# Optimization experiments

Hardware: AMD Instinct MI355X
Metric: run time of the kernel (lower is better)

Reference implementation:

```python
import jax, jax.numpy as jnp
import numpy as np

S = 8192          # total tokens (8 images x 1024 patches)
DIM = 1280        # hidden_size
H = 16            # num_heads
DH = DIM // H     # head_dim = 80
N_SEG = 8         # number of image segments (equal-length)


def setup_inputs() -> dict:
    key = jax.random.key(0)
    ks = jax.random.split(key, 8)
    hidden_states = jax.random.normal(ks[0], (S, DIM), dtype=jnp.float32)
    ang = jax.random.uniform(ks[1], (S, DH), dtype=jnp.float32) * (2.0 * np.pi)
    cos = jnp.cos(ang)
    sin = jnp.sin(ang)
    cu_seqlens = (jnp.arange(N_SEG + 1, dtype=jnp.int32) * (S // N_SEG))
    qkv_w = jax.random.normal(ks[2], (3 * DIM, DIM), dtype=jnp.float32) * 0.02
    qkv_b = jax.random.normal(ks[3], (3 * DIM,), dtype=jnp.float32) * 0.02
    proj_w = jax.random.normal(ks[4], (DIM, DIM), dtype=jnp.float32) * 0.02
    proj_b = jax.random.normal(ks[5], (DIM,), dtype=jnp.float32) * 0.02
    return {
        "hidden_states": hidden_states,
        "cos": cos,
        "sin": sin,
        "qkv_w": qkv_w,
        "qkv_b": qkv_b,
        "proj_w": proj_w,
        "proj_b": proj_b,
        "cu_seqlens": cu_seqlens,
    }


def _rotate_half(x):
    d = x.shape[-1] // 2
    return jnp.concatenate([-x[..., d:], x[..., :d]], axis=-1)


def reference(hidden_states, cos, sin, qkv_w, qkv_b, proj_w, proj_b, cu_seqlens):
    s, dim = hidden_states.shape
    dh = cos.shape[-1]
    h = dim // dh
    n_seg = cu_seqlens.shape[0] - 1  # static; segments are equal-length
    L = s // n_seg
    scale = dh ** -0.5

    # fused QKV projection: [S, 3, H, DH]
    qkv = (hidden_states @ qkv_w.T + qkv_b).reshape(s, 3, h, dh)
    q, k, v = qkv[:, 0], qkv[:, 1], qkv[:, 2]

    # RoPE (fp32, broadcast cos/sin over heads)
    cos_b = cos[:, None, :].astype(jnp.float32)
    sin_b = sin[:, None, :].astype(jnp.float32)
    qf, kf = q.astype(jnp.float32), k.astype(jnp.float32)
    q = (qf * cos_b + _rotate_half(qf) * sin_b).astype(q.dtype)
    k = (kf * cos_b + _rotate_half(kf) * sin_b).astype(k.dtype)

    # per-segment (block-diagonal) attention: reshape to [n_seg, L, H, DH]
    qs = q.reshape(n_seg, L, h, dh)
    ks = k.reshape(n_seg, L, h, dh)
    vs = v.reshape(n_seg, L, h, dh)
    scores = jnp.einsum("glhd,gmhd->ghlm", qs, ks) * scale
    attn = jax.nn.softmax(scores, axis=-1)
    out = jnp.einsum("ghlm,gmhd->glhd", attn, vs).reshape(s, dim)
    return out @ proj_w.T + proj_b
```

## Files before the change

### kernel.cpp

```cpp
#include <hip/hip_runtime.h>
#include <hip/hip_bf16.h>
#include <stdint.h>

typedef unsigned short u16;
typedef unsigned int u32;
typedef __attribute__((ext_vector_type(8))) short short8;
typedef __attribute__((ext_vector_type(4))) float f32x4;

#define DEV __device__ __forceinline__

constexpr int S = 8192;
constexpr int DIM = 1280;
constexpr int H = 16;
constexpr int DH = 80;
constexpr int LSEG = 1024;
constexpr int QKVN = 3 * DIM;
constexpr float SCALE = 0.11180339887498949f * 1.4426950408889634f;

DEV u16 f2bf(float f) {
  u32 u = __float_as_uint(f);
  return (u16)((u + 0x7FFFu + ((u >> 16) & 1u)) >> 16);
}
DEV float bf2f(u16 h) { return __uint_as_float(((u32)h) << 16); }
DEV u32 pkbf(float a, float b) {
  __hip_bfloat162 t = __float22bfloat162_rn(float2{a, b});
  u32 r; __builtin_memcpy(&r, &t, 4); return r;
}

DEV void glds16(const void* g, void* l) {
  __builtin_amdgcn_global_load_lds((__attribute__((address_space(1))) void*)g,
                                   (__attribute__((address_space(3))) void*)l,
                                   16, 0, 0);
}
DEV f32x4 mfma16(short8 a, short8 b, f32x4 c) {
  return __builtin_amdgcn_mfma_f32_16x16x32_bf16(a, b, c, 0, 0, 0);
}

__global__ __launch_bounds__(256) void cvt_kernel(
    const float* __restrict__ X, const float* __restrict__ Wq,
    const float* __restrict__ Wp, u16* __restrict__ Xb,
    u16* __restrict__ Wqb, u16* __restrict__ Wpb) {
  size_t i = ((size_t)blockIdx.x * 256 + threadIdx.x) * 4;
  const size_t n1 = (size_t)S * DIM;
  const size_t n2 = (size_t)QKVN * DIM;
  const size_t n3 = (size_t)DIM * DIM;
  const float* src; u16* dst; size_t off;
  if (i < n1)                { src = X;  dst = Xb;  off = i; }
  else if (i < n1 + n2)      { src = Wq; dst = Wqb; off = i - n1; }
  else if (i < n1 + n2 + n3) { src = Wp; dst = Wpb; off = i - n1 - n2; }
  else return;
  float4 v = *(const float4*)(src + off);
  ushort4 r;
  r.x = f2bf(v.x); r.y = f2bf(v.y); r.z = f2bf(v.z); r.w = f2bf(v.w);
  *(ushort4*)(dst + off) = r;
}

__global__ __launch_bounds__(256) void rope_kernel(
    const u16* __restrict__ QKV, const float* __restrict__ cosp,
    const float* __restrict__ sinp, u16* __restrict__ Qp, u16* __restrict__ Kp) {
  int idx = blockIdx.x * 256 + threadIdx.x;
  int c = idx % 5;
  int sh = idx / 5;
  int s = sh >> 4, h = sh & 15;
  const size_t gbase = (size_t)s * QKVN + h * DH + c * 8;
  const size_t pbase = (size_t)sh * 96 + c * 8;
  short8 q0 = *(const short8*)&QKV[gbase];
  short8 q1 = *(const short8*)&QKV[gbase + 40];
  short8 k0 = *(const short8*)&QKV[gbase + DIM];
  short8 k1 = *(const short8*)&QKV[gbase + DIM + 40];
  float4 ca0 = *(const float4*)&cosp[s * DH + c * 8];
  float4 ca1 = *(const float4*)&cosp[s * DH + c * 8 + 4];
  float4 cb0 = *(const float4*)&cosp[s * DH + c * 8 + 40];
  float4 cb1 = *(const float4*)&cosp[s * DH + c * 8 + 44];
  float4 sa0 = *(const float4*)&sinp[s * DH + c * 8];
  float4 sa1 = *(const float4*)&sinp[s * DH + c * 8 + 4];
  float4 sb0 = *(const float4*)&sinp[s * DH + c * 8 + 40];
  float4 sb1 = *(const float4*)&sinp[s * DH + c * 8 + 44];
  float ca[8] = {ca0.x, ca0.y, ca0.z, ca0.w, ca1.x, ca1.y, ca1.z, ca1.w};
  float cb[8] = {cb0.x, cb0.y, cb0.z, cb0.w, cb1.x, cb1.y, cb1.z, cb1.w};
  float sa[8] = {sa0.x, sa0.y, sa0.z, sa0.w, sa1.x, sa1.y, sa1.z, sa1.w};
  float sb[8] = {sb0.x, sb0.y, sb0.z, sb0.w, sb1.x, sb1.y, sb1.z, sb1.w};
  short8 qo0, qo1, ko0, ko1;
#pragma unroll
  for (int j = 0; j < 8; j++) {
    float qa = bf2f((u16)q0[j]), qb = bf2f((u16)q1[j]);
    float ka = bf2f((u16)k0[j]), kb = bf2f((u16)k1[j]);
    qo0[j] = (short)f2bf((qa * ca[j] - qb * sa[j]) * SCALE);
    qo1[j] = (short)f2bf((qb * cb[j] + qa * sb[j]) * SCALE);
    ko0[j] = (short)f2bf(ka * ca[j] - kb * sa[j]);
    ko1[j] = (short)f2bf(kb * cb[j] + ka * sb[j]);
  }
  *(short8*)&Qp[pbase]      = qo0;
  *(short8*)&Qp[pbase + 40] = qo1;
  *(short8*)&Kp[pbase]      = ko0;
  *(short8*)&Kp[pbase + 40] = ko1;
  if (c == 0) {
    short8 z = {};
    *(short8*)&Qp[pbase + 80] = z; *(short8*)&Qp[pbase + 88] = z;
    *(short8*)&Kp[pbase + 80] = z; *(short8*)&Kp[pbase + 88] = z;
  }
}

__global__ __launch_bounds__(256) void vtrans_kernel(
    const u16* __restrict__ QKV, u16* __restrict__ Vt) {
  __shared__ u16 Ls[64 * 88];
  const int s0 = blockIdx.x * 64, h = blockIdx.y;
  const int tid = threadIdx.x;
  for (int cc = tid; cc < 640; cc += 256) {
    int row = cc / 10, c = cc % 10;
    short8 v = *(const short8*)&QKV[(size_t)(s0 + row) * QKVN + 2 * DIM + h * 80 + c * 8];
    *(short8*)&Ls[row * 88 + c * 8] = v;
  }
  __syncthreads();
  for (int cc = tid; cc < 640; cc += 256) {
    int d = cc / 8, sc = cc % 8;
    u16 tmp[8];
#pragma unroll
    for (int j = 0; j < 8; j++) {
      int op = sc * 8 + j;
      int key = ((op & 3) << 4) + (op >> 2);
      tmp[j] = Ls[key * 88 + d];
    }
    *(short8*)&Vt[(size_t)(h * 80 + d) * S + s0 + sc * 8] = *(short8*)tmp;
  }
}

template <bool OUT_F32>
__global__ __launch_bounds__(512, 2) void gemm_bt(
    const u16* __restrict__ A, const u16* __restrict__ B,
    const float* __restrict__ bias, void* __restrict__ C, int K, int N) {
  __shared__ u16 As[2][2][8192];
  __shared__ u16 Bs[2][2][8192];
  const int ntn = N >> 8;
  const int q = gridDim.x >> 3;
  const int widx = (blockIdx.x & 7) * q + (blockIdx.x >> 3);
  const int m0 = (widx / ntn) << 8;
  const int n0 = (widx % ntn) << 8;
  const int tid = threadIdx.x;
  const int w = tid >> 6, lane = tid & 63;
  const int quad = lane >> 4, l16 = lane & 15;
  const int wm = w >> 2, wn = w & 3;

  const int rowoff = w * 8 + (lane >> 3);
  const int coloff = ((lane & 7) ^ (lane >> 3)) * 8;
  const u16* pa0 = A + (size_t)(m0 + rowoff) * K + coloff;
  const u16* pa1 = A + (size_t)(m0 + 128 + rowoff) * K + coloff;
  const u16* pb0 = B + (size_t)(n0 + rowoff) * K + coloff;
  const u16* pb1 = B + (size_t)(n0 + 128 + rowoff) * K + coloff;
  const size_t j64 = (size_t)64 * K;

#define STG(P, DST, kk) do { \
    glds16((P) + (kk), &(DST)[w * 512]); \
    glds16((P) + j64 + (kk), &(DST)[4096 + w * 512]); } while (0)
#define BARR()  __builtin_amdgcn_s_barrier()
#define SCHED0() __builtin_amdgcn_sched_barrier(0)

  const int aro = (wm * 16 + l16) * 64;
  const int bro = (wn * 16 + l16) * 64;
  const int kc0 = ((quad) ^ (l16 & 7)) * 8;
  const int kc1 = ((4 + quad) ^ (l16 & 7)) * 8;

  f32x4 acc[8][4] = {};
  short8 af[4][2], bf0[2][2], bf1[2][2];
  const int NT = K >> 6;

  STG(pa0, As[0][0], 0); STG(pb0, Bs[0][0], 0);
  STG(pb1, Bs[0][1], 0);
  STG(pa1, As[0][1], 0);
  asm volatile("s_waitcnt vmcnt(2)");
  BARR();
#pragma unroll
  for (int jj = 0; jj < 2; jj++) {
    bf0[jj][0] = *(const short8*)&Bs[0][0][bro + jj * 4096 + kc0];
    bf0[jj][1] = *(const short8*)&Bs[0][0][bro + jj * 4096 + kc1];
  }

  for (int t = 0; t < NT; ++t) {
    const int b = t & 1;
    const int kk = (t + 1) << 6;
    const bool pf = (t + 1 < NT);
#pragma unroll
    for (int i = 0; i < 4; i++) {
      af[i][0] = *(const short8*)&As[b][0][aro + i * 2048 + kc0];
      af[i][1] = *(const short8*)&As[b][0][aro + i * 2048 + kc1];
    }
#pragma unroll
    for (int jj = 0; jj < 2; jj++) {
      bf1[jj][0] = *(const short8*)&Bs[b][1][bro + jj * 4096 + kc0];
      bf1[jj][1] = *(const short8*)&Bs[b][1][bro + jj * 4096 + kc1];
    }
    if (pf) { STG(pa0, As[b ^ 1][0], kk); STG(pb0, Bs[b ^ 1][0], kk); }
    asm volatile("s_waitcnt lgkmcnt(4)");
    SCHED0();
    __builtin_amdgcn_s_setprio(1);
#pragma unroll
    for (int ks = 0; ks < 2; ks++)
#pragma unroll
      for (int i = 0; i < 4; i++)
#pragma unroll
        for (int jj = 0; jj < 2; jj++)
          acc[i][jj] = mfma16(af[i][ks], bf0[jj][ks], acc[i][jj]);
    __builtin_amdgcn_s_setprio(0);
    SCHED0();
    if (pf) asm volatile("s_waitcnt vmcnt(4)");
    else    asm volatile("s_waitcnt vmcnt(0)");
    BARR();
    asm volatile("s_waitcnt lgkmcnt(0)");
    SCHED0();
    if (pf) STG(pb1, Bs[b ^ 1][1], kk);
    __builtin_amdgcn_s_setprio(1);
#pragma unroll
    for (int i = 0; i < 4; i++) {
      acc[i][2] = mfma16(af[i][0], bf1[0][0], acc[i][2]);
      acc[i][3] = mfma16(af[i][0], bf1[1][0], acc[i][3]);
      acc[i][2] = mfma16(af[i][1], bf1[0][1], acc[i][2]);
      acc[i][3] = mfma16(af[i][1], bf1[1][1], acc[i][3]);
      af[i][0] = *(const short8*)&As[b][1][aro + i * 2048 + kc0];
      af[i][1] = *(const short8*)&As[b][1][aro + i * 2048 + kc1];
    }
    __builtin_amdgcn_s_setprio(0);
    if (pf) STG(pa1, As[b ^ 1][1], kk);
    asm volatile("s_waitcnt lgkmcnt(0)");
    SCHED0();
    __builtin_amdgcn_s_setprio(1);
#pragma unroll
    for (int ks = 0; ks < 2; ks++)
#pragma unroll
      for (int i = 0; i < 4; i++)
#pragma unroll
        for (int jj = 0; jj < 2; jj++)
          acc[4 + i][jj] = mfma16(af[i][ks], bf0[jj][ks], acc[4 + i][jj]);
    __builtin_amdgcn_s_setprio(0);
    SCHED0();
    if (pf) asm volatile("s_waitcnt vmcnt(2)");
    else    asm volatile("s_waitcnt vmcnt(0)");
    BARR();
    if (pf) {
#pragma unroll
      for (int jj = 0; jj < 2; jj++) {
        bf0[jj][0] = *(const short8*)&Bs[b ^ 1][0][bro + jj * 4096 + kc0];
        bf0[jj][1] = *(const short8*)&Bs[b ^ 1][0][bro + jj * 4096 + kc1];
      }
      SCHED0();
    }
    __builtin_amdgcn_s_setprio(1);
#pragma unroll
    for (int ks = 0; ks < 2; ks++)
#pragma unroll
      for (int i = 0; i < 4; i++)
#pragma unroll
        for (int jj = 0; jj < 2; jj++)
          acc[4 + i][2 + jj] = mfma16(af[i][ks], bf1[jj][ks], acc[4 + i][2 + jj]);
    __builtin_amdgcn_s_setprio(0);
  }
#undef STG
#undef BARR
#undef SCHED0
#pragma unroll
  for (int nf = 0; nf < 4; nf++) {
    int col = n0 + nf * 64 + wn * 16 + l16;
    float bv = bias[col];
#pragma unroll
    for (int mf = 0; mf < 8; mf++) {
#pragma unroll
      for (int r = 0; r < 4; r++) {
        int row = m0 + mf * 32 + wm * 16 + quad * 4 + r;
        float v = acc[mf][nf][r] + bv;
        if (OUT_F32) ((float*)C)[(size_t)row * N + col] = v;
        else         ((u16*)C)[(size_t)row * N + col] = f2bf(v);
      }
    }
  }
}

__global__ __launch_bounds__(256, 2) void attn_kernel(
    const u16* __restrict__ Qp, const u16* __restrict__ Kp,
    const u16* __restrict__ Vt, u16* __restrict__ O) {
  __shared__ u16 Ks[2][64 * 104];
  __shared__ u16 Vs[2][86 * 72];
  __shared__ u16 Ps[4][2][16 * 72];
  const int bid = blockIdx.x;
  const int phi = bid & 7, qt = (bid >> 3) & 7, pj = bid >> 6;
  const int p = pj * 8 + phi;
  const int g = p >> 4, h = p & 15;
  const int tid = threadIdx.x;
  const int w = tid >> 6, lane = tid & 63;
  const int quad = lane >> 4, l16 = lane & 15;

  short8 aq[2][3];
  const size_t qbase = ((size_t)(g * LSEG + qt * 128 + w * 32 + l16)) * 1536 + h * 96;
#pragma unroll
  for (int mt = 0; mt < 2; mt++)
#pragma unroll
    for (int ks = 0; ks < 3; ks++)
      aq[mt][ks] = *(const short8*)&Qp[qbase + (size_t)mt * 16 * 1536 + ks * 32 + quad * 8];

  const u16* gp[7]; u16* lp0[7]; u16* lp1[7]; int stp[7]; bool act[7];
#pragma unroll
  for (int i = 0; i < 7; i++) {
    int c = w + 4 * i;
    act[i] = (c < 25);
    int cc = act[i] ? c : 0;
    if (cc < 13) {
      int idx = cc * 64 + lane;
      int key = idx / 13, rc = idx % 13;
      int col = rc * 8; if (col >= 96) col = 0;
      gp[i] = Kp + (size_t)(g * LSEG + key) * 1536 + h * 96 + col;
      stp[i] = 64 * 1536;
      lp0[i] = &Ks[0][cc * 512]; lp1[i] = &Ks[1][cc * 512];
    } else {
      int cv = cc - 13;
      int idx = cv * 64 + lane;
      int d = idx / 9, rc = idx % 9;
      int col = rc * 8; if (col >= 64) col = 0;
      if (d >= 80) d = 0;
      gp[i] = Vt + (size_t)(h * 80 + d) * S + g * LSEG + col;
      stp[i] = 64;
      lp0[i] = &Vs[0][cv * 512]; lp1[i] = &Vs[1][cv * 512];
    }
  }
#pragma unroll
  for (int i = 0; i < 7; i++)
    if (act[i]) { glds16(gp[i], lp0[i]); gp[i] += stp[i]; }

  f32x4 o[2][5] = {};
  float lr[2][4] = {};

  for (int kb = 0; kb < LSEG / 64; kb++) {
    const int b = kb & 1;
    __syncthreads();
    if (kb < LSEG / 64 - 1) {
      if (b == 0) {
#pragma unroll
        for (int i = 0; i < 7; i++)
          if (act[i]) { glds16(gp[i], lp1[i]); gp[i] += stp[i]; }
      } else {
#pragma unroll
        for (int i = 0; i < 7; i++)
          if (act[i]) { glds16(gp[i], lp0[i]); gp[i] += stp[i]; }
      }
    }
    f32x4 s[2][4] = {};
#pragma unroll
    for (int ks = 0; ks < 3; ks++) {
      short8 bk[4];
#pragma unroll
      for (int nt = 0; nt < 4; nt++)
        bk[nt] = *(const short8*)&Ks[b][(nt * 16 + l16) * 104 + ks * 32 + quad * 8];
#pragma unroll
      for (int mt = 0; mt < 2; mt++)
#pragma unroll
        for (int nt = 0; nt < 4; nt++)
          s[mt][nt] = mfma16(aq[mt][ks], bk[nt], s[mt][nt]);
    }
    short8 vb[5][2];
#pragma unroll
    for (int t = 0; t < 5; t++)
#pragma unroll
      for (int u = 0; u < 2; u++)
        vb[t][u] = *(const short8*)&Vs[b][(t * 16 + l16) * 72 + u * 32 + quad * 8];
#pragma unroll
    for (int mt = 0; mt < 2; mt++) {
      u16* psw = &Ps[w][mt][0];
#pragma unroll
      for (int r = 0; r < 4; r++) {
        float p0 = __builtin_amdgcn_exp2f(s[mt][0][r]);
        float p1 = __builtin_amdgcn_exp2f(s[mt][1][r]);
        float p2 = __builtin_amdgcn_exp2f(s[mt][2][r]);
        float p3 = __builtin_amdgcn_exp2f(s[mt][3][r]);
        lr[mt][r] += (p0 + p1) + (p2 + p3);
        int row = quad * 4 + r;
        uint2 pk; pk.x = pkbf(p0, p1); pk.y = pkbf(p2, p3);
        *(uint2*)&psw[row * 72 + l16 * 4] = pk;
      }
    }
    short8 pa[2][2];
#pragma unroll
    for (int mt = 0; mt < 2; mt++) {
      pa[mt][0] = *(const short8*)&Ps[w][mt][l16 * 72 + quad * 8];
      pa[mt][1] = *(const short8*)&Ps[w][mt][l16 * 72 + 32 + quad * 8];
    }
#pragma unroll
    for (int mt = 0; mt < 2; mt++) {
#pragma unroll
      for (int t = 0; t < 5; t++)
        o[mt][t] = mfma16(pa[mt][0], vb[t][0], o[mt][t]);
#pragma unroll
      for (int t = 0; t < 5; t++)
        o[mt][t] = mfma16(pa[mt][1], vb[t][1], o[mt][t]);
    }
  }
#pragma unroll
  for (int mt = 0; mt < 2; mt++)
#pragma unroll
    for (int r = 0; r < 4; r++) {
      float t = lr[mt][r];
#pragma unroll
      for (int off = 8; off >= 1; off >>= 1) t += __shfl_xor(t, off, 16);
      float inv = 1.f / t;
      int srow = g * LSEG + qt * 128 + w * 32 + mt * 16 + quad * 4 + r;
#pragma unroll
      for (int tt = 0; tt < 5; tt++)
        O[(size_t)srow * DIM + h * DH + tt * 16 + l16] = f2bf(o[mt][tt][r] * inv);
    }
}

extern "C" void kernel_launch(void* const* d_in, const int* in_sizes, int n_in,
                              void* d_out, int out_size, void* d_ws, size_t ws_size,
                              hipStream_t stream) {
  const float* X     = (const float*)d_in[0];
  const float* cosp  = (const float*)d_in[1];
  const float* sinp  = (const float*)d_in[2];
  const float* qkvw  = (const float*)d_in[3];
  const float* qkvb  = (const float*)d_in[4];
  const float* projw = (const float*)d_in[5];
  const float* projb = (const float*)d_in[6];
  float* out = (float*)d_out;

  u16* Xb   = (u16*)d_ws;
  u16* Wqb  = Xb   + (size_t)S * DIM;
  u16* Wpb  = Wqb  + (size_t)QKVN * DIM;
  u16* QKVb = Wpb  + (size_t)DIM * DIM;
  u16* Kp   = QKVb + (size_t)S * QKVN;
  u16* Vt   = Kp   + (size_t)S * H * 96;
  u16* Qp   = Xb;
  u16* AOb  = QKVb;

  cvt_kernel<<<16640, 256, 0, stream>>>(X, qkvw, projw, Xb, Wqb, Wpb);
  gemm_bt<false><<<(S / 256) * (QKVN / 256), 512, 0, stream>>>(Xb, Wqb, qkvb, QKVb, DIM, QKVN);
  rope_kernel<<<(S * H * 5) / 256, 256, 0, stream>>>(QKVb, cosp, sinp, Qp, Kp);
  vtrans_kernel<<<dim3(S / 64, H), 256, 0, stream>>>(QKVb, Vt);
  attn_kernel<<<1024, 256, 0, stream>>>(Qp, Kp, Vt, AOb);
  gemm_bt<true><<<(S / 256) * (DIM / 256), 512, 0, stream>>>(AOb, Wpb, projb, out, DIM, DIM);
}
```

Before: 328.9 us.

## Fuse RoPE and V transpose into QKV GEMM epilogue via permuted weight rows

Moves the RoPE and the V-transpose work into the QKV GEMM epilogue. The Q/K weight rows are permuted during conversion so each rotate-half pair lands in adjacent lanes, where __shfl_xor can combine them. The epilogue then stages results through LDS and writes padded Qp/Kp and the transposed Vt directly. This removes two kernel launches and the round trip of the full QKV buffer through global memory, at the cost of a heavier GEMM epilogue with extra cos/sin loads and LDS syncs. The cvt kernel also zeroes the Q/K padding.

```diff
diff --git a/kernel.cpp b/kernel.cpp
--- a/kernel.cpp
+++ b/kernel.cpp
@@ -39,96 +39,54 @@
 __global__ __launch_bounds__(256) void cvt_kernel(
     const float* __restrict__ X, const float* __restrict__ Wq,
     const float* __restrict__ Wp, u16* __restrict__ Xb,
-    u16* __restrict__ Wqb, u16* __restrict__ Wpb) {
+    u16* __restrict__ Wqb, u16* __restrict__ Wpb,
+    u16* __restrict__ Qp, u16* __restrict__ Kp) {
   size_t i = ((size_t)blockIdx.x * 256 + threadIdx.x) * 4;
   const size_t n1 = (size_t)S * DIM;
   const size_t n2 = (size_t)QKVN * DIM;
   const size_t n3 = (size_t)DIM * DIM;
-  const float* src; u16* dst; size_t off;
-  if (i < n1)                { src = X;  dst = Xb;  off = i; }
-  else if (i < n1 + n2)      { src = Wq; dst = Wqb; off = i - n1; }
-  else if (i < n1 + n2 + n3) { src = Wp; dst = Wpb; off = i - n1 - n2; }
-  else return;
-  float4 v = *(const float4*)(src + off);
-  ushort4 r;
-  r.x = f2bf(v.x); r.y = f2bf(v.y); r.z = f2bf(v.z); r.w = f2bf(v.w);
-  *(ushort4*)(dst + off) = r;
-}
-
-__global__ __launch_bounds__(256) void rope_kernel(
-    const u16* __restrict__ QKV, const float* __restrict__ cosp,
-    const float* __restrict__ sinp, u16* __restrict__ Qp, u16* __restrict__ Kp) {
-  int idx = blockIdx.x * 256 + threadIdx.x;
-  int c = idx % 5;
-  int sh = idx / 5;
-  int s = sh >> 4, h = sh & 15;
-  const size_t gbase = (size_t)s * QKVN + h * DH + c * 8;
-  const size_t pbase = (size_t)sh * 96 + c * 8;
-  short8 q0 = *(const short8*)&QKV[gbase];
-  short8 q1 = *(const short8*)&QKV[gbase + 40];
-  short8 k0 = *(const short8*)&QKV[gbase + DIM];
-  short8 k1 = *(const short8*)&QKV[gbase + DIM + 40];
-  float4 ca0 = *(const float4*)&cosp[s * DH + c * 8];
-  float4 ca1 = *(const float4*)&cosp[s * DH + c * 8 + 4];
-  float4 cb0 = *(const float4*)&cosp[s * DH + c * 8 + 40];
-  float4 cb1 = *(const float4*)&cosp[s * DH + c * 8 + 44];
-  float4 sa0 = *(const float4*)&sinp[s * DH + c * 8];
-  float4 sa1 = *(const float4*)&sinp[s * DH + c * 8 + 4];
-  float4 sb0 = *(const float4*)&sinp[s * DH + c * 8 + 40];
-  float4 sb1 = *(const float4*)&sinp[s * DH + c * 8 + 44];
-  float ca[8] = {ca0.x, ca0.y, ca0.z, ca0.w, ca1.x, ca1.y, ca1.z, ca1.w};
-  float cb[8] = {cb0.x, cb0.y, cb0.z, cb0.w, cb1.x, cb1.y, cb1.z, cb1.w};
-  float sa[8] = {sa0.x, sa0.y, sa0.z, sa0.w, sa1.x, sa1.y, sa1.z, sa1.w};
-  float sb[8] = {sb0.x, sb0.y, sb0.z, sb0.w, sb1.x, sb1.y, sb1.z, sb1.w};
-  short8 qo0, qo1, ko0, ko1;
-#pragma unroll
-  for (int j = 0; j < 8; j++) {
-    float qa = bf2f((u16)q0[j]), qb = bf2f((u16)q1[j]);
-    float ka = bf2f((u16)k0[j]), kb = bf2f((u16)k1[j]);
-    qo0[j] = (short)f2bf((qa * ca[j] - qb * sa[j]) * SCALE);
-    qo1[j] = (short)f2bf((qb * cb[j] + qa * sb[j]) * SCALE);
-    ko0[j] = (short)f2bf(ka * ca[j] - kb * sa[j]);
-    ko1[j] = (short)f2bf(kb * cb[j] + ka * sb[j]);
-  }
-  *(short8*)&Qp[pbase]      = qo0;
-  *(short8*)&Qp[pbase + 40] = qo1;
-  *(short8*)&Kp[pbase]      = ko0;
-  *(short8*)&Kp[pbase + 40] = ko1;
-  if (c == 0) {
-    short8 z = {};
-    *(short8*)&Qp[pbase + 80] = z; *(short8*)&Qp[pbase + 88] = z;
-    *(short8*)&Kp[pbase + 80] = z; *(short8*)&Kp[pbase + 88] = z;
-  }
-}
-
-__global__ __launch_bounds__(256) void vtrans_kernel(
-    const u16* __restrict__ QKV, u16* __restrict__ Vt) {
-  __shared__ u16 Ls[64 * 88];
-  const int s0 = blockIdx.x * 64, h = blockIdx.y;
-  const int tid = threadIdx.x;
-  for (int cc = tid; cc < 640; cc += 256) {
-    int row = cc / 10, c = cc % 10;
-    short8 v = *(const short8*)&QKV[(size_t)(s0 + row) * QKVN + 2 * DIM + h * 80 + c * 8];
-    *(short8*)&Ls[row * 88 + c * 8] = v;
-  }
-  __syncthreads();
-  for (int cc = tid; cc < 640; cc += 256) {
-    int d = cc / 8, sc = cc % 8;
-    u16 tmp[8];
-#pragma unroll
-    for (int j = 0; j < 8; j++) {
-      int op = sc * 8 + j;
-      int key = ((op & 3) << 4) + (op >> 2);
-      tmp[j] = Ls[key * 88 + d];
-    }
-    *(short8*)&Vt[(size_t)(h * 80 + d) * S + s0 + sc * 8] = *(short8*)tmp;
-  }
-}
-
-template <bool OUT_F32>
+  const size_t n123 = n1 + n2 + n3;
+  if (i < n1) {
+    float4 v = *(const float4*)(X + i);
+    ushort4 r; r.x = f2bf(v.x); r.y = f2bf(v.y); r.z = f2bf(v.z); r.w = f2bf(v.w);
+    *(ushort4*)(Xb + i) = r;
+  } else if (i < n1 + n2) {
+    size_t off = i - n1;
+    int row = (int)(off / DIM), col = (int)(off % DIM);
+    int drow = row;
+    if (row < 2560) {
+      int i80 = row % 80;
+      int p = (i80 < 40) ? 2 * i80 : 2 * (i80 - 40) + 1;
+      drow = row - i80 + p;
+    }
+    float4 v = *(const float4*)(Wq + off);
+    ushort4 r; r.x = f2bf(v.x); r.y = f2bf(v.y); r.z = f2bf(v.z); r.w = f2bf(v.w);
+    *(ushort4*)(Wqb + (size_t)drow * DIM + col) = r;
+  } else if (i < n123) {
+    size_t off = i - n1 - n2;
+    float4 v = *(const float4*)(Wp + off);
+    ushort4 r; r.x = f2bf(v.x); r.y = f2bf(v.y); r.z = f2bf(v.z); r.w = f2bf(v.w);
+    *(ushort4*)(Wpb + off) = r;
+  } else {
+    size_t j = (i - n123) >> 2;
+    size_t f = j * 8;
+    const size_t half = (size_t)S * H * 16;
+    if (f < 2 * half) {
+      u16* base = (f < half) ? Qp : Kp;
+      size_t rem = (f < half) ? f : f - half;
+      size_t sh = rem >> 4; int o16 = (int)(rem & 15);
+      short8 z = {};
+      *(short8*)&base[sh * 96 + 80 + o16] = z;
+    }
+  }
+}
+
+template <int MODE>
 __global__ __launch_bounds__(512, 2) void gemm_bt(
     const u16* __restrict__ A, const u16* __restrict__ B,
-    const float* __restrict__ bias, void* __restrict__ C, int K, int N) {
+    const float* __restrict__ bias, void* __restrict__ C, int K, int N,
+    const float* __restrict__ cosp, const float* __restrict__ sinp,
+    u16* __restrict__ Qp, u16* __restrict__ Kp, u16* __restrict__ Vt) {
   __shared__ u16 As[2][2][8192];
   __shared__ u16 Bs[2][2][8192];
   const int ntn = N >> 8;
@@ -256,18 +214,103 @@
 #undef STG
 #undef BARR
 #undef SCHED0
-#pragma unroll
-  for (int nf = 0; nf < 4; nf++) {
-    int col = n0 + nf * 64 + wn * 16 + l16;
-    float bv = bias[col];
-#pragma unroll
-    for (int mf = 0; mf < 8; mf++) {
-#pragma unroll
-      for (int r = 0; r < 4; r++) {
-        int row = m0 + mf * 32 + wm * 16 + quad * 4 + r;
-        float v = acc[mf][nf][r] + bv;
-        if (OUT_F32) ((float*)C)[(size_t)row * N + col] = v;
-        else         ((u16*)C)[(size_t)row * N + col] = f2bf(v);
+  if (MODE == 1) {
+#pragma unroll
+    for (int nf = 0; nf < 4; nf++) {
+      int col = n0 + nf * 64 + wn * 16 + l16;
+      float bv = bias[col];
+#pragma unroll
+      for (int mf = 0; mf < 8; mf++)
+#pragma unroll
+        for (int r = 0; r < 4; r++) {
+          int row = m0 + mf * 32 + wm * 16 + quad * 4 + r;
+          ((float*)C)[(size_t)row * N + col] = acc[mf][nf][r] + bv;
+        }
+    }
+  } else {
+    const int tn = n0 >> 8;
+    u16* Lbuf = &As[0][0][0];
+    asm volatile("s_waitcnt lgkmcnt(0)");
+    __syncthreads();
+    if (tn < 10) {
+      const bool isQ = (tn < 5);
+      const int secQK = isQ ? 0 : 1280;
+      u16* dst = isQ ? Qp : Kp;
+#pragma unroll
+      for (int hc = 0; hc < 2; hc++) {
+        if (hc) __syncthreads();
+#pragma unroll
+        for (int nf2 = 0; nf2 < 2; nf2++) {
+          const int nf = hc * 2 + nf2;
+          const int c = n0 + nf * 64 + wn * 16 + l16;
+          const int rel = c - secQK;
+          const int h = rel / 80, i80 = rel % 80;
+          const int uu = i80 & 1, pr_ = i80 >> 1;
+          const int d = pr_ + uu * 40;
+          const float bv = bias[secQK + h * 80 + d];
+          const int lc = nf2 * 64 + wn * 16 + l16;
+#pragma unroll
+          for (int mf = 0; mf < 8; mf++) {
+#pragma unroll
+            for (int r = 0; r < 4; r++) {
+              const int s = m0 + mf * 32 + wm * 16 + quad * 4 + r;
+              float v = acc[mf][nf][r] + bv;
+              float pv = __shfl_xor(v, 1);
+              float cv = cosp[s * 80 + d], sv = sinp[s * 80 + d];
+              float out = (uu == 0) ? (v * cv - pv * sv) : (v * cv + pv * sv);
+              if (isQ) out *= SCALE;
+              Lbuf[(mf * 32 + wm * 16 + quad * 4 + r) * 128 + lc] = f2bf(out);
+            }
+          }
+        }
+        __syncthreads();
+        const int W = (n0 - secQK) + hc * 128;
+#pragma unroll
+        for (int j = 0; j < 8; j++) {
+          int cc = j * 512 + tid;
+          int s = cc >> 4, ci = cc & 15;
+          int gi = ci >> 1, uu = ci & 1;
+          int gb = W + gi * 16;
+          int h = gb / 80;
+          int d0 = (gb % 80) / 2 + uu * 40;
+          u16 tmp[8];
+#pragma unroll
+          for (int t2 = 0; t2 < 8; t2++)
+            tmp[t2] = Lbuf[s * 128 + gi * 16 + uu + 2 * t2];
+          *(short8*)&dst[((size_t)(m0 + s) * 16 + h) * 96 + d0] = *(short8*)tmp;
+        }
+      }
+    } else {
+#pragma unroll
+      for (int hc = 0; hc < 2; hc++) {
+        if (hc) __syncthreads();
+#pragma unroll
+        for (int nf2 = 0; nf2 < 2; nf2++) {
+          const int nf = hc * 2 + nf2;
+          const float bv = bias[n0 + nf * 64 + wn * 16 + l16];
+          const int lc = nf2 * 64 + wn * 16 + l16;
+#pragma unroll
+          for (int mf = 0; mf < 8; mf++)
+#pragma unroll
+            for (int r = 0; r < 4; r++)
+              Lbuf[(mf * 32 + wm * 16 + quad * 4 + r) * 128 + lc] =
+                  f2bf(acc[mf][nf][r] + bv);
+        }
+        __syncthreads();
+        const int Wv = (n0 - 2560) + hc * 128;
+#pragma unroll
+        for (int j = 0; j < 8; j++) {
+          int cc = j * 512 + tid;
+          int lc = cc >> 5, g4 = (cc >> 3) & 3, sc = cc & 7;
+          u16 tmp[8];
+#pragma unroll
+          for (int t2 = 0; t2 < 8; t2++) {
+            int op = sc * 8 + t2;
+            int key = ((op & 3) << 4) + (op >> 2);
+            tmp[t2] = Lbuf[(g4 * 64 + key) * 128 + lc];
+          }
+          *(short8*)&Vt[(size_t)(Wv + lc) * S + m0 + g4 * 64 + sc * 8] = *(short8*)tmp;
+        }
       }
     }
   }
@@ -420,16 +463,15 @@
   u16* Xb   = (u16*)d_ws;
   u16* Wqb  = Xb   + (size_t)S * DIM;
   u16* Wpb  = Wqb  + (size_t)QKVN * DIM;
-  u16* QKVb = Wpb  + (size_t)DIM * DIM;
-  u16* Kp   = QKVb + (size_t)S * QKVN;
+  u16* Qp   = Wpb  + (size_t)DIM * DIM;
+  u16* Kp   = Qp   + (size_t)S * H * 96;
   u16* Vt   = Kp   + (size_t)S * H * 96;
-  u16* Qp   = Xb;
-  u16* AOb  = QKVb;
-
-  cvt_kernel<<<16640, 256, 0, stream>>>(X, qkvw, projw, Xb, Wqb, Wpb);
-  gemm_bt<false><<<(S / 256) * (QKVN / 256), 512, 0, stream>>>(Xb, Wqb, qkvb, QKVb, DIM, QKVN);
-  rope_kernel<<<(S * H * 5) / 256, 256, 0, stream>>>(QKVb, cosp, sinp, Qp, Kp);
-  vtrans_kernel<<<dim3(S / 64, H), 256, 0, stream>>>(QKVb, Vt);
+  u16* AOb  = Xb;
+
+  cvt_kernel<<<18688, 256, 0, stream>>>(X, qkvw, projw, Xb, Wqb, Wpb, Qp, Kp);
+  gemm_bt<0><<<(S / 256) * (QKVN / 256), 512, 0, stream>>>(
+      Xb, Wqb, qkvb, nullptr, DIM, QKVN, cosp, sinp, Qp, Kp, Vt);
   attn_kernel<<<1024, 256, 0, stream>>>(Qp, Kp, Vt, AOb);
-  gemm_bt<true><<<(S / 256) * (DIM / 256), 512, 0, stream>>>(AOb, Wpb, projb, out, DIM, DIM);
-}
+  gemm_bt<1><<<(S / 256) * (DIM / 256), 512, 0, stream>>>(
+      AOb, Wpb, projb, out, DIM, DIM, nullptr, nullptr, nullptr, nullptr, nullptr);
+}
```

After: 352.1 us. 1.07x slower.
